# Performance work log

Measured on AMD Instinct MI355X. Metric: run time of the kernel, lower is better.

## Reference

```python
import jax, jax.numpy as jnp
import numpy as np

B, C, H, W, K = 16, 1, 768, 768, 512


def setup_inputs() -> dict:
    key = jax.random.key(0)
    k1, k2, k3 = jax.random.split(key, 3)
    pre_denses = jax.random.normal(k1, (B, C, H, W), dtype=jnp.float32)
    gt_denses = jax.random.normal(k2, (B, C, H, W), dtype=jnp.float32)
    gt_cors = jax.random.randint(k3, (B, K, 2), 0, min(H, W), dtype=jnp.int32)
    return {"pre_denses": pre_denses, "gt_denses": gt_denses, "gt_cors": gt_cors}


def _peak_mask(pre):
    # The original pads by 2, shift-compares, then crops by 1; this is equivalent
    # to a zero-pad-by-1 4-neighbor local-max test at every original pixel.
    p = jnp.pad(pre, ((0, 0), (0, 0), (1, 1), (1, 1)))
    left = p[:, :, 1:-1, 2:]
    right = p[:, :, 1:-1, :-2]
    up = p[:, :, 2:, 1:-1]
    down = p[:, :, :-2, 1:-1]
    return (pre > left) & (pre > right) & (pre > up) & (pre > down)


def reference(pre_denses, gt_denses, gt_cors):
    b, c, h, w = pre_denses.shape
    # --- loss1: peak-position loss ---
    pre_mask = _peak_mask(pre_denses)  # [B,1,H,W] bool
    batch_idx = jnp.arange(b)[:, None]           # [B,1]
    ys = gt_cors[:, :, 1]                        # row index
    xs = gt_cors[:, :, 0]                        # col index
    gt_mask = jnp.zeros((b, c, h, w), dtype=bool).at[batch_idx, 0, ys, xs].set(True)
    mask1 = jnp.bitwise_xor(pre_mask, gt_mask).astype(jnp.float32)  # C_head = 1
    error = (pre_denses - gt_denses) ** 2
    l1 = jnp.mean(jnp.sum(mask1 * error, axis=(1, 2, 3)))
    # --- loss2: weighted MSE ---
    head = (gt_denses > 0).astype(jnp.float32)
    mse_mask = 5.0 * head + (1.0 - head)  # C_head=5, C_no_head=1
    l2 = jnp.mean(jnp.sum(mse_mask * error, axis=(1, 2, 3)))
    return l1 + l2
```

## Files before the change

### kernel.cpp

```cpp
#include <hip/hip_runtime.h>

#define BDIM 16
#define HDIM 768
#define WDIM 768
#define KCOR 512
#define STRIP 16
constexpr int HW = HDIM * WDIM;
constexpr int QW = WDIM / 4;
constexpr int STRIPS = HDIM / STRIP;

__global__ __launch_bounds__(QW) void main_kernel(
    const float* __restrict__ pre,
    const float* __restrict__ gt,
    float* __restrict__ out) {

    const int b     = blockIdx.x / STRIPS;
    const int strip = blockIdx.x % STRIPS;
    const int r0    = strip * STRIP;
    const int t     = threadIdx.x;

    const float* preb = pre + b * HW;
    const float* gtb  = gt  + b * HW;

    int idx = r0 * WDIM + t * 4;

    float4 u4 = (r0 > 0) ? *(const float4*)(preb + idx - WDIM)
                         : make_float4(0.f, 0.f, 0.f, 0.f);
    float4 c4 = *(const float4*)(preb + idx);

    float acc = 0.0f;
    #pragma unroll 4
    for (int r = 0; r < STRIP; ++r) {
        const int row = r0 + r;
        const float4 d4 = (row < HDIM - 1) ? *(const float4*)(preb + idx + WDIM)
                                           : make_float4(0.f, 0.f, 0.f, 0.f);
        const float4 g4 = *(const float4*)(gtb + idx);
        const float lft = (t > 0)      ? preb[idx - 1] : 0.0f;
        const float rgt = (t < QW - 1) ? preb[idx + 4] : 0.0f;

        const float c[4]  = {c4.x, c4.y, c4.z, c4.w};
        const float g[4]  = {g4.x, g4.y, g4.z, g4.w};
        const float u[4]  = {u4.x, u4.y, u4.z, u4.w};
        const float d[4]  = {d4.x, d4.y, d4.z, d4.w};
        const float lr[6] = {lft, c[0], c[1], c[2], c[3], rgt};

        #pragma unroll
        for (int j = 0; j < 4; ++j) {
            const bool peak = (c[j] > lr[j]) && (c[j] > lr[j + 2]) &&
                              (c[j] > u[j]) && (c[j] > d[j]);
            float e = c[j] - g[j];
            e *= e;
            const float wt = (g[j] > 0.0f ? 5.0f : 1.0f) + (peak ? 1.0f : 0.0f);
            acc += wt * e;
        }

        u4 = c4;
        c4 = d4;
        idx += WDIM;
    }

    #pragma unroll
    for (int off = 32; off > 0; off >>= 1) acc += __shfl_down(acc, off);

    __shared__ float lds[3];
    const int wave = threadIdx.x >> 6;
    const int lane = threadIdx.x & 63;
    if (lane == 0) lds[wave] = acc;
    __syncthreads();
    if (threadIdx.x == 0) {
        atomicAdd(out, (lds[0] + lds[1] + lds[2]) * (1.0f / (float)BDIM));
    }
}

__global__ __launch_bounds__(KCOR) void corr_kernel(
    const float* __restrict__ pre,
    const float* __restrict__ gt,
    const int* __restrict__ cors,
    float* __restrict__ out) {

    __shared__ int scoord[KCOR];
    const int b = blockIdx.x;
    const int k = threadIdx.x;
    const int x = cors[(b * KCOR + k) * 2 + 0];
    const int y = cors[(b * KCOR + k) * 2 + 1];
    const int packed = y * WDIM + x;
    scoord[k] = packed;
    __syncthreads();

    bool dup = false;
    for (int k2 = 0; k2 < k; ++k2) dup |= (scoord[k2] == packed);

    float contrib = 0.0f;
    if (!dup) {
        const int idx = b * HW + packed;
        const float c = pre[idx];
        const float l = (x > 0)        ? pre[idx - 1]    : 0.0f;
        const float r = (x < WDIM - 1) ? pre[idx + 1]    : 0.0f;
        const float u = (y > 0)        ? pre[idx - WDIM] : 0.0f;
        const float d = (y < HDIM - 1) ? pre[idx + WDIM] : 0.0f;
        const bool peak = (c > l) && (c > r) && (c > u) && (c > d);
        float e = c - gt[idx];
        e *= e;
        contrib = (peak ? -1.0f : 1.0f) * e;
    }

    #pragma unroll
    for (int off = 32; off > 0; off >>= 1) contrib += __shfl_down(contrib, off);

    __shared__ float lds[8];
    const int wave = threadIdx.x >> 6;
    const int lane = threadIdx.x & 63;
    if (lane == 0) lds[wave] = contrib;
    __syncthreads();
    if (threadIdx.x == 0) {
        float s = 0.0f;
        #pragma unroll
        for (int i = 0; i < 8; ++i) s += lds[i];
        atomicAdd(out, s * (1.0f / (float)BDIM));
    }
}

extern "C" void kernel_launch(void* const* d_in, const int* in_sizes, int n_in,
                              void* d_out, int out_size, void* d_ws, size_t ws_size,
                              hipStream_t stream) {
    const float* pre  = (const float*)d_in[0];
    const float* gt   = (const float*)d_in[1];
    const int*   cors = (const int*)d_in[2];

    float* out = (float*)d_out;

    hipMemsetAsync(out, 0, sizeof(float), stream);

    main_kernel<<<BDIM * STRIPS, QW, 0, stream>>>(pre, gt, out);

    corr_kernel<<<BDIM, KCOR, 0, stream>>>(pre, gt, cors, out);
}
```

Measured before the change: 116.7 us.

## Fuse correction pass into main kernel and dedupe coordinates with LDS hash table

The separate correction kernel is merged into the strip-reduction kernel: the first BDIM blocks handle the ground-truth coordinate correction and the rest do the dense weighted-error sweep, all in one launch. Duplicate coordinates are now found with an LDS open-addressing hash table built with atomicCAS, replacing the quadratic scan over earlier entries. This removes one kernel launch and its tail gap and lets the correction work overlap the streaming pass. The cost is extra shared memory per block and some divergence inside the correction blocks.

New measurement: 111.1 us. -4.8%, faster.

```diff
diff --git a/kernel.cpp b/kernel.cpp
--- a/kernel.cpp
+++ b/kernel.cpp
@@ -8,115 +8,110 @@
 constexpr int HW = HDIM * WDIM;
 constexpr int QW = WDIM / 4;
 constexpr int STRIPS = HDIM / STRIP;
+constexpr int NSTRIPB = BDIM * STRIPS;
+constexpr int NCORRB = BDIM;
+constexpr int NBLK = NSTRIPB + NCORRB;
 
-__global__ __launch_bounds__(QW) void main_kernel(
+__global__ __launch_bounds__(QW) void fused_kernel(
     const float* __restrict__ pre,
     const float* __restrict__ gt,
+    const int* __restrict__ cors,
     float* __restrict__ out) {
 
-    const int b     = blockIdx.x / STRIPS;
-    const int strip = blockIdx.x % STRIPS;
-    const int r0    = strip * STRIP;
-    const int t     = threadIdx.x;
-
-    const float* preb = pre + b * HW;
-    const float* gtb  = gt  + b * HW;
-
-    int idx = r0 * WDIM + t * 4;
-
-    float4 u4 = (r0 > 0) ? *(const float4*)(preb + idx - WDIM)
-                         : make_float4(0.f, 0.f, 0.f, 0.f);
-    float4 c4 = *(const float4*)(preb + idx);
+    __shared__ int   table[1024];
+    __shared__ float red[3];
 
     float acc = 0.0f;
-    #pragma unroll 4
-    for (int r = 0; r < STRIP; ++r) {
-        const int row = r0 + r;
-        const float4 d4 = (row < HDIM - 1) ? *(const float4*)(preb + idx + WDIM)
-                                           : make_float4(0.f, 0.f, 0.f, 0.f);
-        const float4 g4 = *(const float4*)(gtb + idx);
-        const float lft = (t > 0)      ? preb[idx - 1] : 0.0f;
-        const float rgt = (t < QW - 1) ? preb[idx + 4] : 0.0f;
 
-        const float c[4]  = {c4.x, c4.y, c4.z, c4.w};
-        const float g[4]  = {g4.x, g4.y, g4.z, g4.w};
-        const float u[4]  = {u4.x, u4.y, u4.z, u4.w};
-        const float d[4]  = {d4.x, d4.y, d4.z, d4.w};
-        const float lr[6] = {lft, c[0], c[1], c[2], c[3], rgt};
+    if (blockIdx.x >= NCORRB) {
+        const int sid   = blockIdx.x - NCORRB;
+        const int b     = sid / STRIPS;
+        const int strip = sid % STRIPS;
+        const int r0    = strip * STRIP;
+        const int t     = threadIdx.x;
 
-        #pragma unroll
-        for (int j = 0; j < 4; ++j) {
-            const bool peak = (c[j] > lr[j]) && (c[j] > lr[j + 2]) &&
-                              (c[j] > u[j]) && (c[j] > d[j]);
-            float e = c[j] - g[j];
-            e *= e;
-            const float wt = (g[j] > 0.0f ? 5.0f : 1.0f) + (peak ? 1.0f : 0.0f);
-            acc += wt * e;
+        const float* preb = pre + b * HW;
+        const float* gtb  = gt  + b * HW;
+
+        int idx = r0 * WDIM + t * 4;
+
+        float4 u4 = (r0 > 0) ? *(const float4*)(preb + idx - WDIM)
+                             : make_float4(0.f, 0.f, 0.f, 0.f);
+        float4 c4 = *(const float4*)(preb + idx);
+
+        #pragma unroll 4
+        for (int r = 0; r < STRIP; ++r) {
+            const int row = r0 + r;
+            const float4 d4 = (row < HDIM - 1) ? *(const float4*)(preb + idx + WDIM)
+                                               : make_float4(0.f, 0.f, 0.f, 0.f);
+            const float4 g4 = *(const float4*)(gtb + idx);
+            const float lft = (t > 0)      ? preb[idx - 1] : 0.0f;
+            const float rgt = (t < QW - 1) ? preb[idx + 4] : 0.0f;
+
+            const float c[4]  = {c4.x, c4.y, c4.z, c4.w};
+            const float g[4]  = {g4.x, g4.y, g4.z, g4.w};
+            const float u[4]  = {u4.x, u4.y, u4.z, u4.w};
+            const float d[4]  = {d4.x, d4.y, d4.z, d4.w};
+            const float lr[6] = {lft, c[0], c[1], c[2], c[3], rgt};
+
+            #pragma unroll
+            for (int j = 0; j < 4; ++j) {
+                const bool peak = (c[j] > lr[j]) && (c[j] > lr[j + 2]) &&
+                                  (c[j] > u[j]) && (c[j] > d[j]);
+                float e = c[j] - g[j];
+                e *= e;
+                const float wt = (g[j] > 0.0f ? 5.0f : 1.0f) + (peak ? 1.0f : 0.0f);
+                acc += wt * e;
+            }
+
+            u4 = c4;
+            c4 = d4;
+            idx += WDIM;
         }
+    } else {
+        const int b = blockIdx.x;
 
-        u4 = c4;
-        c4 = d4;
-        idx += WDIM;
+        for (int i = threadIdx.x; i < 1024; i += QW) table[i] = -1;
+        __syncthreads();
+
+        for (int k = threadIdx.x; k < KCOR; k += QW) {
+            const int x = cors[(b * KCOR + k) * 2 + 0];
+            const int y = cors[(b * KCOR + k) * 2 + 1];
+            const int packed = y * WDIM + x;
+
+            unsigned h = ((unsigned)packed * 2654435761u) >> 22;
+            bool mine = false;
+            for (;;) {
+                const int old = atomicCAS(&table[h], -1, packed);
+                if (old == -1)     { mine = true; break; }
+                if (old == packed) { break; }
+                h = (h + 1) & 1023;
+            }
+
+            if (mine) {
+                const int idx = b * HW + packed;
+                const float c = pre[idx];
+                const float l = (x > 0)        ? pre[idx - 1]    : 0.0f;
+                const float r = (x < WDIM - 1) ? pre[idx + 1]    : 0.0f;
+                const float u = (y > 0)        ? pre[idx - WDIM] : 0.0f;
+                const float d = (y < HDIM - 1) ? pre[idx + WDIM] : 0.0f;
+                const bool peak = (c > l) && (c > r) && (c > u) && (c > d);
+                float e = c - gt[idx];
+                e *= e;
+                acc += (peak ? -1.0f : 1.0f) * e;
+            }
+        }
     }
 
     #pragma unroll
     for (int off = 32; off > 0; off >>= 1) acc += __shfl_down(acc, off);
 
-    __shared__ float lds[3];
     const int wave = threadIdx.x >> 6;
     const int lane = threadIdx.x & 63;
-    if (lane == 0) lds[wave] = acc;
+    if (lane == 0) red[wave] = acc;
     __syncthreads();
     if (threadIdx.x == 0) {
-        atomicAdd(out, (lds[0] + lds[1] + lds[2]) * (1.0f / (float)BDIM));
-    }
-}
-
-__global__ __launch_bounds__(KCOR) void corr_kernel(
-    const float* __restrict__ pre,
-    const float* __restrict__ gt,
-    const int* __restrict__ cors,
-    float* __restrict__ out) {
-
-    __shared__ int scoord[KCOR];
-    const int b = blockIdx.x;
-    const int k = threadIdx.x;
-    const int x = cors[(b * KCOR + k) * 2 + 0];
-    const int y = cors[(b * KCOR + k) * 2 + 1];
-    const int packed = y * WDIM + x;
-    scoord[k] = packed;
-    __syncthreads();
-
-    bool dup = false;
-    for (int k2 = 0; k2 < k; ++k2) dup |= (scoord[k2] == packed);
-
-    float contrib = 0.0f;
-    if (!dup) {
-        const int idx = b * HW + packed;
-        const float c = pre[idx];
-        const float l = (x > 0)        ? pre[idx - 1]    : 0.0f;
-        const float r = (x < WDIM - 1) ? pre[idx + 1]    : 0.0f;
-        const float u = (y > 0)        ? pre[idx - WDIM] : 0.0f;
-        const float d = (y < HDIM - 1) ? pre[idx + WDIM] : 0.0f;
-        const bool peak = (c > l) && (c > r) && (c > u) && (c > d);
-        float e = c - gt[idx];
-        e *= e;
-        contrib = (peak ? -1.0f : 1.0f) * e;
-    }
-
-    #pragma unroll
-    for (int off = 32; off > 0; off >>= 1) contrib += __shfl_down(contrib, off);
-
-    __shared__ float lds[8];
-    const int wave = threadIdx.x >> 6;
-    const int lane = threadIdx.x & 63;
-    if (lane == 0) lds[wave] = contrib;
-    __syncthreads();
-    if (threadIdx.x == 0) {
-        float s = 0.0f;
-        #pragma unroll
-        for (int i = 0; i < 8; ++i) s += lds[i];
-        atomicAdd(out, s * (1.0f / (float)BDIM));
+        atomicAdd(out, (red[0] + red[1] + red[2]) * (1.0f / (float)BDIM));
     }
 }
 
@@ -131,7 +126,5 @@
 
     hipMemsetAsync(out, 0, sizeof(float), stream);
 
-    main_kernel<<<BDIM * STRIPS, QW, 0, stream>>>(pre, gt, out);
-
-    corr_kernel<<<BDIM, KCOR, 0, stream>>>(pre, gt, cors, out);
+    fused_kernel<<<NBLK, QW, 0, stream>>>(pre, gt, cors, out);
 }
```
